# Performance work log

Measured on AMD Instinct MI355X. Metric: run time of the kernel, lower is better.

## Reference

```python
import jax, jax.numpy as jnp
import numpy as np

HIDDEN = 2048
HEADS = 16
HEAD_DIM = HIDDEN // HEADS

def setup_inputs() -> dict:
    key = jax.random.key(0)
    ks = jax.random.split(key, 9)
    B, S = 1, 4096
    scale = 1.0 / np.sqrt(HIDDEN)
    x = jax.random.normal(ks[0], (B, S, HIDDEN), dtype=jnp.float32)
    Wq = jax.random.normal(ks[1], (HIDDEN, HIDDEN), dtype=jnp.float32) * scale
    Wk = jax.random.normal(ks[2], (HIDDEN, HIDDEN), dtype=jnp.float32) * scale
    Wv = jax.random.normal(ks[3], (HIDDEN, HIDDEN), dtype=jnp.float32) * scale
    Wo = jax.random.normal(ks[4], (HIDDEN, HIDDEN), dtype=jnp.float32) * scale
    bq = jax.random.normal(ks[5], (HIDDEN,), dtype=jnp.float32) * 0.01
    bk = jax.random.normal(ks[6], (HIDDEN,), dtype=jnp.float32) * 0.01
    bv = jax.random.normal(ks[7], (HIDDEN,), dtype=jnp.float32) * 0.01
    bo = jax.random.normal(ks[8], (HIDDEN,), dtype=jnp.float32) * 0.01
    return {"x": x, "Wq": Wq, "bq": bq, "Wk": Wk, "bk": bk, "Wv": Wv, "bv": bv, "Wo": Wo, "bo": bo}

def reference(x, Wq, bq, Wk, bk, Wv, bv, Wo, bo):
    B, S, D = x.shape
    H, Hd = HEADS, HEAD_DIM
    # projections (nn.Linear: x @ W^T + b)
    Q = (x @ Wq.T + bq).reshape(B, S, H, Hd).transpose(0, 2, 1, 3)  # [B,H,S,Hd]
    K = (x @ Wk.T + bk).reshape(B, S, H, Hd).transpose(0, 2, 1, 3)
    V = (x @ Wv.T + bv).reshape(B, S, H, Hd).transpose(0, 2, 1, 3)
    scores = jnp.einsum('bhqd,bhkd->bhqk', Q, K) / jnp.sqrt(jnp.float32(Hd))
    attn = jax.nn.softmax(scores, axis=-1)
    out = jnp.einsum('bhqk,bhkd->bhqd', attn, V)  # [B,H,S,Hd]
    out = out.transpose(0, 2, 1, 3).reshape(B, S, D)
    return out @ Wo.T + bo
```

## Files before the change

### kernel.cpp

```cpp
#include <hip/hip_runtime.h>

#define S_LEN  4096
#define DMODEL 2048
#define NHEADS 16
#define HDIM   128

typedef __bf16 bf16x8 __attribute__((ext_vector_type(8)));
typedef __bf16 bf16x2 __attribute__((ext_vector_type(2)));
typedef float  f32x4  __attribute__((ext_vector_type(4)));
typedef float  f32x16 __attribute__((ext_vector_type(16)));

__device__ __forceinline__ unsigned short f2b(float f) {
    unsigned int u = __float_as_uint(f);
    unsigned int r = (u + 0x7fffu + ((u >> 16) & 1u)) >> 16;
    return (unsigned short)r;
}

__device__ __forceinline__ unsigned int pkbf16(float a, float b) {
#if __has_builtin(__builtin_amdgcn_cvt_pk_bf16_f32)
    bf16x2 t = __builtin_amdgcn_cvt_pk_bf16_f32(a, b);
    return *(unsigned int*)&t;
#else
    return (unsigned int)f2b(a) | ((unsigned int)f2b(b) << 16);
#endif
}

__device__ __forceinline__ f32x4 mfma16(bf16x8 a, bf16x8 b, f32x4 c) {
    return __builtin_amdgcn_mfma_f32_16x16x32_bf16(a, b, c, 0, 0, 0);
}

__device__ __forceinline__ f32x16 mfma32(bf16x8 a, bf16x8 b, f32x16 c) {
    return __builtin_amdgcn_mfma_f32_32x32x16_bf16(a, b, c, 0, 0, 0);
}

__device__ __forceinline__ void ldg2lds16(const void* g, void* l) {
    __builtin_amdgcn_global_load_lds(
        (__attribute__((address_space(1))) void*)(void*)g,
        (__attribute__((address_space(3))) void*)l, 16, 0, 0);
}

__global__ __launch_bounds__(256) void cvt_bf16(
    const float* __restrict__ src, unsigned short* __restrict__ dst, int n4)
{
    int i = blockIdx.x * blockDim.x + threadIdx.x;
    if (i < n4) {
        float4 v = ((const float4*)src)[i];
        uint2 h;
        h.x = pkbf16(v.x, v.y); h.y = pkbf16(v.z, v.w);
        ((uint2*)dst)[i] = h;
    }
}

__global__ __launch_bounds__(256) void cvt_bf16_w4(
    const float* __restrict__ w0, const float* __restrict__ w1,
    const float* __restrict__ w2, const float* __restrict__ w3,
    unsigned short* __restrict__ d0, unsigned short* __restrict__ d1,
    unsigned short* __restrict__ d2, unsigned short* __restrict__ d3)
{
    const int z = blockIdx.y;
    const float* src = (z == 0) ? w0 : (z == 1) ? w1 : (z == 2) ? w2 : w3;
    unsigned short* dst = (z == 0) ? d0 : (z == 1) ? d1 : (z == 2) ? d2 : d3;
    int i = blockIdx.x * blockDim.x + threadIdx.x;
    float4 v = ((const float4*)src)[i];
    uint2 h;
    h.x = pkbf16(v.x, v.y); h.y = pkbf16(v.z, v.w);
    ((uint2*)dst)[i] = h;
}

#define GBM 256
#define GBN 128
#define GBK 64
#define GNT (DMODEL / GBK)

#define G_STAGE(Abase, Bbase, Amat, Bmat, kt)                                  \
    {                                                                          \
        const int srow = lane >> 3;                                            \
        const int gc = (lane & 7) ^ (srow & 7);                                \
        _Pragma("unroll")                                                      \
        for (int j2 = 0; j2 < 4; j2++) {                                       \
            int r = w * 32 + j2 * 8 + srow;                                    \
            ldg2lds16(&(Amat)[(size_t)(m0 + r) * DMODEL + (kt) * GBK + gc * 8],\
                      &(Abase)[(w * 32 + j2 * 8) * GBK]);                      \
        }                                                                      \
        _Pragma("unroll")                                                      \
        for (int j2 = 0; j2 < 2; j2++) {                                       \
            int r = w * 16 + j2 * 8 + srow;                                    \
            ldg2lds16(&(Bmat)[(size_t)(n0 + r) * DMODEL + (kt) * GBK + gc * 8],\
                      &(Bbase)[(w * 16 + j2 * 8) * GBK]);                      \
        }                                                                      \
    }

#define G_COMPUTE(Abase, Bbase)                                                \
    {                                                                          \
        _Pragma("unroll")                                                      \
        for (int kk = 0; kk < 2; kk++) {                                       \
            bf16x8 af[4], bfr[4];                                              \
            _Pragma("unroll")                                                  \
            for (int i = 0; i < 4; i++)                                        \
                af[i] = *(const bf16x8*)                                       \
                    &(Abase)[(wm + i * 16 + lo) * GBK +                        \
                             (((kk * 4 + qd) ^ (lo & 7)) * 8)];                \
            _Pragma("unroll")                                                  \
            for (int j = 0; j < 4; j++)                                        \
                bfr[j] = *(const bf16x8*)                                      \
                    &(Bbase)[(wn + j * 16 + lo) * GBK +                        \
                             (((kk * 4 + qd) ^ (lo & 7)) * 8)];                \
            __builtin_amdgcn_s_setprio(1);                                     \
            _Pragma("unroll")                                                  \
            for (int i = 0; i < 4; i++)                                        \
                _Pragma("unroll")                                              \
                for (int j = 0; j < 4; j++)                                    \
                    acc[i][j] = mfma16(af[i], bfr[j], acc[i][j]);              \
            __builtin_amdgcn_s_setprio(0);                                     \
        }                                                                      \
    }

#define G_MAIN_LOOP(Amat, Bmat)                                                \
    G_STAGE(sA[0], sB[0], Amat, Bmat, 0);                                      \
    G_STAGE(sA[1], sB[1], Amat, Bmat, 1);                                      \
    asm volatile("s_waitcnt vmcnt(6)" ::: "memory");                           \
    __builtin_amdgcn_s_barrier();                                              \
    {                                                                          \
        int c = 0;                                                             \
        for (int t = 0; t < GNT; ++t) {                                        \
            int cn = c + 2; if (cn >= 3) cn -= 3;                              \
            if (t + 2 < GNT) G_STAGE(sA[cn], sB[cn], Amat, Bmat, t + 2);       \
            G_COMPUTE(sA[c], sB[c]);                                           \
            if (t + 2 < GNT)                                                   \
                asm volatile("s_waitcnt vmcnt(6)" ::: "memory");               \
            else                                                               \
                asm volatile("s_waitcnt vmcnt(0)" ::: "memory");               \
            __builtin_amdgcn_s_barrier();                                      \
            if (++c >= 3) c = 0;                                               \
        }                                                                      \
    }

__global__ __launch_bounds__(512, 2) void gemm_qkv(
    const unsigned short* __restrict__ xb,
    const unsigned short* __restrict__ Wqb, const float* __restrict__ bq,
    const unsigned short* __restrict__ Wkb, const float* __restrict__ bk,
    const unsigned short* __restrict__ Wvb, const float* __restrict__ bv,
    unsigned short* __restrict__ Qb, unsigned short* __restrict__ Kb,
    unsigned short* __restrict__ Vb)
{
    const int z = blockIdx.z;
    const unsigned short* B = (z == 0) ? Wqb : (z == 1) ? Wkb : Wvb;
    const float* bias        = (z == 0) ? bq  : (z == 1) ? bk  : bv;
    unsigned short* C        = (z == 0) ? Qb  : (z == 1) ? Kb  : Vb;
    const float oscale = (z == 0) ? 0.12751743f : 1.0f;

    __shared__ alignas(16) unsigned short smem[3 * (GBM + GBN) * GBK];
    unsigned short* sA[3]; unsigned short* sB[3];
#pragma unroll
    for (int i = 0; i < 3; i++) {
        sA[i] = smem + i * (GBM + GBN) * GBK;
        sB[i] = sA[i] + GBM * GBK;
    }

    const int tid = threadIdx.x;
    const int w = tid >> 6, lane = tid & 63, lo = lane & 15, qd = lane >> 4;
    const int wm = (w >> 1) * 64, wn = (w & 1) * 64;
    const int m0 = blockIdx.y * GBM, n0 = blockIdx.x * GBN;

    f32x4 acc[4][4] = {};

    G_MAIN_LOOP(xb, B);

#pragma unroll
    for (int j = 0; j < 4; j++) {
        int n = n0 + wn + j * 16 + lo;
        float bv_ = bias[n];
#pragma unroll
        for (int i = 0; i < 4; i++) {
#pragma unroll
            for (int r = 0; r < 4; r++) {
                int m = m0 + wm + i * 16 + qd * 4 + r;
                C[(size_t)m * DMODEL + n] = f2b((acc[i][j][r] + bv_) * oscale);
            }
        }
    }
}

__global__ __launch_bounds__(512, 2) void gemm_out(
    const unsigned short* __restrict__ Aatt, const unsigned short* __restrict__ Wob,
    const float* __restrict__ bo, float* __restrict__ out)
{
    __shared__ alignas(16) unsigned short smem[3 * (GBM + GBN) * GBK];
    unsigned short* sA[3]; unsigned short* sB[3];
#pragma unroll
    for (int i = 0; i < 3; i++) {
        sA[i] = smem + i * (GBM + GBN) * GBK;
        sB[i] = sA[i] + GBM * GBK;
    }

    const int tid = threadIdx.x;
    const int w = tid >> 6, lane = tid & 63, lo = lane & 15, qd = lane >> 4;
    const int wm = (w >> 1) * 64, wn = (w & 1) * 64;
    const int m0 = blockIdx.y * GBM, n0 = blockIdx.x * GBN;

    f32x4 acc[4][4] = {};

    G_MAIN_LOOP(Aatt, Wob);

#pragma unroll
    for (int j = 0; j < 4; j++) {
        int n = n0 + wn + j * 16 + lo;
        float bv_ = bo[n];
#pragma unroll
        for (int i = 0; i < 4; i++) {
#pragma unroll
            for (int r = 0; r < 4; r++) {
                int m = m0 + wm + i * 16 + qd * 4 + r;
                out[(size_t)m * DMODEL + n] = acc[i][j][r] + bv_;
            }
        }
    }
}

__global__ __launch_bounds__(256) void transpose_v(
    const unsigned short* __restrict__ Vb, unsigned short* __restrict__ Vt)
{
    __shared__ unsigned short tile[64 * 67];
    const int s0 = blockIdx.x * 64;
    const int d0 = blockIdx.y * 64;
    const int tid = threadIdx.x;
#pragma unroll
    for (int i = 0; i < 2; i++) {
        int chunk = tid + i * 256;
        int r = chunk >> 3, c8 = (chunk & 7) * 8;
        uint4 v = *(const uint4*)&Vb[(size_t)(s0 + r) * DMODEL + d0 + c8];
        const unsigned short* p = (const unsigned short*)&v;
#pragma unroll
        for (int j = 0; j < 8; j++) tile[r * 67 + c8 + j] = p[j];
    }
    __syncthreads();
#pragma unroll
    for (int i = 0; i < 2; i++) {
        int chunk = tid + i * 256;
        int r = chunk >> 3, c8 = (chunk & 7) * 8;
        unsigned short tmp[8];
#pragma unroll
        for (int j = 0; j < 8; j++) tmp[j] = tile[(c8 + j) * 67 + r];
        *(uint4*)&Vt[(size_t)(d0 + r) * S_LEN + s0 + c8] = *(uint4*)tmp;
    }
}

__global__ __launch_bounds__(256, 2) void attn_kernel(
    const unsigned short* __restrict__ Qb, const unsigned short* __restrict__ Kb,
    const unsigned short* __restrict__ Vt, unsigned short* __restrict__ Ob)
{
    const int id = blockIdx.x;
    const int xcd = id & 7, slot = id >> 3;
    const int h  = (xcd << 1) | (slot >> 6);
    const int q0 = (slot & 63) * 64;

    __shared__ alignas(16) unsigned char smem[66048];
    unsigned short* Ks0  = (unsigned short*)smem;
    unsigned short* Vts0 = (unsigned short*)(smem + 16384);
    unsigned short* Ks1  = (unsigned short*)(smem + 32768);
    unsigned short* Vts1 = (unsigned short*)(smem + 49152);
    float* Of = (float*)smem;
    float* Lf = (float*)(smem + 65536);

    const int tid = threadIdx.x;
    const int w = tid >> 6, lane = tid & 63;
    const int qw = w >> 1, kw = w & 1;
    const int l31 = lane & 31, hi = lane >> 5;
    const int sw7 = l31 & 7;

    bf16x8 qf[8];
    {
        const unsigned short* qrow =
            &Qb[(size_t)(q0 + qw * 32 + l31) * DMODEL + h * HDIM];
#pragma unroll
        for (int sl = 0; sl < 8; sl++)
            qf[sl] = *(const bf16x8*)&qrow[sl * 16 + hi * 8];
    }

    f32x16 o_acc[4] = {};
    float l_run = 0.f;

    const int krow = kw * 32 + l31;

#define STAGE_K(dst_, key0_)                                                  \
    {                                                                         \
        _Pragma("unroll")                                                     \
        for (int i = 0; i < 4; i++) {                                         \
            int r = w * 16 + i * 4 + (lane >> 4);                             \
            int c = (lane & 15) ^ (r & 7);                                    \
            ldg2lds16(&Kb[(size_t)((key0_) + r) * DMODEL + h * HDIM + c * 8], \
                      &(dst_)[(w * 16 + i * 4) * 128]);                       \
        }                                                                     \
    }
#define STAGE_V(dst_, key0_)                                                  \
    {                                                                         \
        _Pragma("unroll")                                                     \
        for (int i = 0; i < 4; i++) {                                         \
            int r = w * 32 + i * 8 + (lane >> 3);                             \
            int c = (lane & 7) ^ (r & 7);                                     \
            ldg2lds16(&Vt[(size_t)(h * HDIM + r) * S_LEN + (key0_) + c * 8],  \
                      &(dst_)[(w * 32 + i * 8) * 64]);                        \
        }                                                                     \
    }

#define ATTN_ITER(KsC, VtsC, KsN, VtsN, kbn)                                  \
    {                                                                         \
        if ((kbn) < S_LEN / 64) {                                             \
            STAGE_K(KsN, (kbn) * 64);                                         \
            STAGE_V(VtsN, (kbn) * 64);                                        \
        }                                                                     \
        f32x16 s = {};                                                        \
        __builtin_amdgcn_s_setprio(1);                                        \
        _Pragma("unroll")                                                     \
        for (int sl = 0; sl < 8; sl++) {                                      \
            bf16x8 kf = *(const bf16x8*)                                      \
                &(KsC)[krow * 128 + (((2 * sl + hi) ^ sw7) * 8)];             \
            s = mfma32(kf, qf[sl], s);                                        \
        }                                                                     \
        __builtin_amdgcn_s_setprio(0);                                        \
        bf16x8 pa0, pa1;                                                      \
        {                                                                     \
            float ls = 0.f;                                                   \
            _Pragma("unroll")                                                 \
            for (int k2 = 0; k2 < 2; k2++) {                                  \
                float e0 = __builtin_amdgcn_exp2f(s[8 * k2 + 0]);             \
                float e1 = __builtin_amdgcn_exp2f(s[8 * k2 + 1]);             \
                float e2 = __builtin_amdgcn_exp2f(s[8 * k2 + 2]);             \
                float e3 = __builtin_amdgcn_exp2f(s[8 * k2 + 3]);             \
                float e4 = __builtin_amdgcn_exp2f(s[8 * k2 + 4]);             \
                float e5 = __builtin_amdgcn_exp2f(s[8 * k2 + 5]);             \
                float e6 = __builtin_amdgcn_exp2f(s[8 * k2 + 6]);             \
                float e7 = __builtin_amdgcn_exp2f(s[8 * k2 + 7]);             \
                ls += ((e0 + e1) + (e2 + e3)) + ((e4 + e5) + (e6 + e7));      \
                unsigned int c0 = pkbf16(e0, e1);                             \
                unsigned int c1 = pkbf16(e2, e3);                             \
                unsigned int c2 = pkbf16(e4, e5);                             \
                unsigned int c3 = pkbf16(e6, e7);                             \
                asm("v_permlane32_swap_b32 %0, %1" : "+v"(c0), "+v"(c2));     \
                asm("v_permlane32_swap_b32 %0, %1" : "+v"(c1), "+v"(c3));     \
                uint4 u; u.x = c0; u.y = c1; u.z = c2; u.w = c3;              \
                if (k2 == 0) pa0 = *(bf16x8*)&u; else pa1 = *(bf16x8*)&u;     \
            }                                                                 \
            l_run += ls;                                                      \
        }                                                                     \
        __builtin_amdgcn_s_setprio(1);                                        \
        _Pragma("unroll")                                                     \
        for (int k2 = 0; k2 < 2; k2++) {                                      \
            const int gch = 4 * kw + 2 * k2 + hi;                             \
            bf16x8 pf = (k2 == 0) ? pa0 : pa1;                                \
            _Pragma("unroll")                                                 \
            for (int dt = 0; dt < 4; dt++) {                                  \
                bf16x8 vf = *(const bf16x8*)                                  \
                    &(VtsC)[(dt * 32 + l31) * 64 + ((gch ^ sw7) * 8)];        \
                o_acc[dt] = mfma32(pf, vf, o_acc[dt]);                        \
            }                                                                 \
        }                                                                     \
        __builtin_amdgcn_s_setprio(0);                                        \
        __syncthreads();                                                      \
    }

    STAGE_K(Ks0, 0);
    STAGE_V(Vts0, 0);
    __syncthreads();

    for (int kb = 0; kb < S_LEN / 64; kb += 2) {
        ATTN_ITER(Ks0, Vts0, Ks1, Vts1, kb + 1);
        ATTN_ITER(Ks1, Vts1, Ks0, Vts0, kb + 2);
    }
#undef ATTN_ITER
#undef STAGE_K
#undef STAGE_V

    float l = l_run + __shfl_xor(l_run, 32);

    if (kw == 1) {
#pragma unroll
        for (int dt = 0; dt < 4; dt++)
#pragma unroll
            for (int r = 0; r < 16; r++) {
                int row = (r & 3) + 8 * (r >> 2) + 4 * hi;
                Of[(qw * 32 + row) * 128 + dt * 32 + l31] = o_acc[dt][r];
            }
    }
    if (hi == 0) Lf[(qw * 2 + kw) * 32 + l31] = l;
    __syncthreads();

    if (kw == 0) {
        float linv[16];
#pragma unroll
        for (int r = 0; r < 16; r++) {
            int row = (r & 3) + 8 * (r >> 2) + 4 * hi;
            linv[r] = 1.0f / (Lf[(qw * 2 + 0) * 32 + row] +
                              Lf[(qw * 2 + 1) * 32 + row]);
        }
#pragma unroll
        for (int dt = 0; dt < 4; dt++)
#pragma unroll
            for (int r = 0; r < 16; r++) {
                int row = (r & 3) + 8 * (r >> 2) + 4 * hi;
                float v = o_acc[dt][r] + Of[(qw * 32 + row) * 128 + dt * 32 + l31];
                Ob[(size_t)(q0 + qw * 32 + row) * DMODEL + h * HDIM + dt * 32 + l31]
                    = f2b(v * linv[r]);
            }
    }
}

extern "C" void kernel_launch(void* const* d_in, const int* in_sizes, int n_in,
                              void* d_out, int out_size, void* d_ws, size_t ws_size,
                              hipStream_t stream)
{
    const float* x  = (const float*)d_in[0];
    const float* Wq = (const float*)d_in[1];
    const float* bq = (const float*)d_in[2];
    const float* Wk = (const float*)d_in[3];
    const float* bk = (const float*)d_in[4];
    const float* Wv = (const float*)d_in[5];
    const float* bv = (const float*)d_in[6];
    const float* Wo = (const float*)d_in[7];
    const float* bo = (const float*)d_in[8];
    float* out = (float*)d_out;

    const size_t N = (size_t)S_LEN * DMODEL;
    const size_t W = (size_t)DMODEL * DMODEL;
    unsigned short* Qb  = (unsigned short*)d_ws;
    unsigned short* Kb  = Qb + N;
    unsigned short* Vb  = Kb + N;
    unsigned short* xbv = Vb + N;
    unsigned short* Wqb = xbv + N;
    unsigned short* Wkb = Wqb + W;
    unsigned short* Wvb = Wkb + W;
    unsigned short* Wob = Wvb + W;
    unsigned short* Vt  = xbv;
    unsigned short* Ob  = Vb;

    cvt_bf16<<<(int)(N / 4 / 256), 256, 0, stream>>>(x, xbv, (int)(N / 4));
    cvt_bf16_w4<<<dim3((unsigned)(W / 4 / 256), 4), 256, 0, stream>>>(
        Wq, Wk, Wv, Wo, Wqb, Wkb, Wvb, Wob);

    gemm_qkv<<<dim3(DMODEL / GBN, S_LEN / GBM, 3), 512, 0, stream>>>(
        xbv, Wqb, bq, Wkb, bk, Wvb, bv, Qb, Kb, Vb);

    transpose_v<<<dim3(S_LEN / 64, DMODEL / 64), 256, 0, stream>>>(Vb, Vt);

    attn_kernel<<<1024, 256, 0, stream>>>(Qb, Kb, Vt, Ob);

    gemm_out<<<dim3(DMODEL / GBN, S_LEN / GBM), 512, 0, stream>>>(Ob, Wob, bo, out);
}
```

Measured before the change: 556.2 us.

## Split GEMM K-tile into two phases with interleaved half-stage loads and barriers

```diff
diff --git a/kernel.cpp b/kernel.cpp
--- a/kernel.cpp
+++ b/kernel.cpp
@@ -72,65 +72,78 @@
 #define GBK 64
 #define GNT (DMODEL / GBK)
 
-#define G_STAGE(Abase, Bbase, Amat, Bmat, kt)                                  \
+#define G_STAGE_HALF(ph, Ab, Bb, Amat, Bmat, kt)                               \
     {                                                                          \
         const int srow = lane >> 3;                                            \
-        const int gc = (lane & 7) ^ (srow & 7);                                \
+        const int gc8 = ((lane & 7) ^ (srow & 7)) * 8;                         \
+        const size_t kofs = (size_t)(kt) * GBK + gc8;                          \
         _Pragma("unroll")                                                      \
-        for (int j2 = 0; j2 < 4; j2++) {                                       \
-            int r = w * 32 + j2 * 8 + srow;                                    \
-            ldg2lds16(&(Amat)[(size_t)(m0 + r) * DMODEL + (kt) * GBK + gc * 8],\
-                      &(Abase)[(w * 32 + j2 * 8) * GBK]);                      \
+        for (int L = 0; L < 2; L++) {                                          \
+            int rb = w * 8 + ((ph) * 2 + L) * 64;                              \
+            ldg2lds16(&(Amat)[(size_t)(m0 + rb + srow) * DMODEL + kofs],       \
+                      &(Ab)[rb * GBK]);                                        \
         }                                                                      \
+        {                                                                      \
+            int rb = w * 8 + (ph) * 64;                                        \
+            ldg2lds16(&(Bmat)[(size_t)(n0 + rb + srow) * DMODEL + kofs],       \
+                      &(Bb)[rb * GBK]);                                        \
+        }                                                                      \
+    }
+
+#define G_PHASE(Ac, Bc, kk)                                                    \
+    {                                                                          \
+        bf16x8 af[4], bfr[4];                                                  \
         _Pragma("unroll")                                                      \
-        for (int j2 = 0; j2 < 2; j2++) {                                       \
-            int r = w * 16 + j2 * 8 + srow;                                    \
-            ldg2lds16(&(Bmat)[(size_t)(n0 + r) * DMODEL + (kt) * GBK + gc * 8],\
-                      &(Bbase)[(w * 16 + j2 * 8) * GBK]);                      \
-        }                                                                      \
-    }
-
-#define G_COMPUTE(Abase, Bbase)                                                \
-    {                                                                          \
+        for (int i = 0; i < 4; i++)                                            \
+            af[i] = *(const bf16x8*)                                           \
+                &(Ac)[(wm + i * 16 + lo) * GBK +                               \
+                      ((((kk) * 4 + qd) ^ (lo & 7)) * 8)];                     \
         _Pragma("unroll")                                                      \
-        for (int kk = 0; kk < 2; kk++) {                                       \
-            bf16x8 af[4], bfr[4];                                              \
-            _Pragma("unroll")                                                  \
-            for (int i = 0; i < 4; i++)                                        \
-                af[i] = *(const bf16x8*)                                       \
-                    &(Abase)[(wm + i * 16 + lo) * GBK +                        \
-                             (((kk * 4 + qd) ^ (lo & 7)) * 8)];                \
+        for (int j = 0; j < 4; j++)                                            \
+            bfr[j] = *(const bf16x8*)                                          \
+                &(Bc)[(wn + j * 16 + lo) * GBK +                               \
+                      ((((kk) * 4 + qd) ^ (lo & 7)) * 8)];                     \
+        asm volatile("" ::: "memory");                                         \
+        __builtin_amdgcn_s_barrier();                                          \
+        asm volatile("" ::: "memory");                                         \
+        __builtin_amdgcn_s_setprio(1);                                         \
+        _Pragma("unroll")                                                      \
+        for (int i = 0; i < 4; i++)                                            \
             _Pragma("unroll")                                                  \
             for (int j = 0; j < 4; j++)                                        \
-                bfr[j] = *(const bf16x8*)                                      \
-                    &(Bbase)[(wn + j * 16 + lo) * GBK +                        \
-                             (((kk * 4 + qd) ^ (lo & 7)) * 8)];                \
-            __builtin_amdgcn_s_setprio(1);                                     \
-            _Pragma("unroll")                                                  \
-            for (int i = 0; i < 4; i++)                                        \
-                _Pragma("unroll")                                              \
-                for (int j = 0; j < 4; j++)                                    \
-                    acc[i][j] = mfma16(af[i], bfr[j], acc[i][j]);              \
-            __builtin_amdgcn_s_setprio(0);                                     \
-        }                                                                      \
+                acc[i][j] = mfma16(af[i], bfr[j], acc[i][j]);                  \
+        __builtin_amdgcn_s_setprio(0);                                         \
+    }
+
+#define G_TILE(Ac, Bc, A2, B2, Amat, Bmat, t)                                  \
+    {                                                                          \
+        const bool st_ = (t) + 2 < GNT;                                        \
+        if (st_) G_STAGE_HALF(0, A2, B2, Amat, Bmat, (t) + 2);                 \
+        G_PHASE(Ac, Bc, 0);                                                    \
+        asm volatile("" ::: "memory");                                         \
+        __builtin_amdgcn_s_barrier();                                          \
+        asm volatile("" ::: "memory");                                         \
+        if (st_) G_STAGE_HALF(1, A2, B2, Amat, Bmat, (t) + 2);                 \
+        G_PHASE(Ac, Bc, 1);                                                    \
+        if (st_) asm volatile("s_waitcnt vmcnt(6)" ::: "memory");              \
+        else     asm volatile("s_waitcnt vmcnt(0)" ::: "memory");              \
+        __builtin_amdgcn_s_barrier();                                          \
+        asm volatile("" ::: "memory");                                         \
     }
 
 #define G_MAIN_LOOP(Amat, Bmat)                                                \
-    G_STAGE(sA[0], sB[0], Amat, Bmat, 0);                                      \
-    G_STAGE(sA[1], sB[1], Amat, Bmat, 1);                                      \
+    G_STAGE_HALF(0, sA[0], sB[0], Amat, Bmat, 0);                              \
+    G_STAGE_HALF(1, sA[0], sB[0], Amat, Bmat, 0);                              \
+    G_STAGE_HALF(0, sA[1], sB[1], Amat, Bmat, 1);                              \
+    G_STAGE_HALF(1, sA[1], sB[1], Amat, Bmat, 1);                              \
     asm volatile("s_waitcnt vmcnt(6)" ::: "memory");                           \
     __builtin_amdgcn_s_barrier();                                              \
+    asm volatile("" ::: "memory");                                             \
     {                                                                          \
         int c = 0;                                                             \
         for (int t = 0; t < GNT; ++t) {                                        \
-            int cn = c + 2; if (cn >= 3) cn -= 3;                              \
-            if (t + 2 < GNT) G_STAGE(sA[cn], sB[cn], Amat, Bmat, t + 2);       \
-            G_COMPUTE(sA[c], sB[c]);                                           \
-            if (t + 2 < GNT)                                                   \
-                asm volatile("s_waitcnt vmcnt(6)" ::: "memory");               \
-            else                                                               \
-                asm volatile("s_waitcnt vmcnt(0)" ::: "memory");               \
-            __builtin_amdgcn_s_barrier();                                      \
+            int c2 = c + 2; if (c2 >= 3) c2 -= 3;                              \
+            G_TILE(sA[c], sB[c], sA[c2], sB[c2], Amat, Bmat, t);               \
             if (++c >= 3) c = 0;                                               \
         }                                                                      \
     }
```

Result: slower. 585.7 us (+5.3%).
